# Kernel tuning notes

Measured on AMD Instinct MI355X. Metric: run time of the kernel, lower is better.

The kernel has to match this reference:

```python
import jax, jax.numpy as jnp
import numpy as np

N_NODES = 50000
N_EDGES = 800000
IN_DIM = 64


def setup_inputs() -> dict:
    key = jax.random.key(0)
    ks = jax.random.split(key, 5)
    h = jax.random.normal(ks[0], (N_NODES, IN_DIM), dtype=jnp.float32)
    src = jax.random.randint(ks[1], (N_EDGES,), 0, N_NODES, dtype=jnp.int64 if jax.config.read('jax_enable_x64') else jnp.int32)
    dst = jax.random.randint(ks[2], (N_EDGES,), 0, N_NODES, dtype=src.dtype)
    # attention MLP: Linear(2*in_dim, 1); stored as [2*in_dim, 1] (x @ W + b)
    W_att = jax.random.normal(ks[3], (2 * IN_DIM, 1), dtype=jnp.float32) / np.sqrt(2 * IN_DIM)
    b_att = jnp.zeros((1,), dtype=jnp.float32)
    W_t = jax.random.normal(ks[4], (IN_DIM, IN_DIM), dtype=jnp.float32) / np.sqrt(IN_DIM)
    b_t = jnp.zeros((IN_DIM,), dtype=jnp.float32)
    return {"h": h, "src": src, "dst": dst, "W_att": W_att, "b_att": b_att, "W_t": W_t, "b_t": b_t}


def reference(h, src, dst, W_att, b_att, W_t, b_t):
    h_src = h[src]                                   # [E, D] gather
    h_dst = h[dst]                                   # [E, D] gather
    edge_feat = jnp.concatenate([h_src, h_dst], axis=-1)  # [E, 2D]
    logits = jax.nn.leaky_relu(edge_feat @ W_att + b_att, negative_slope=0.2)[:, 0]  # [E]
    # NOTE: original does softmax over ALL edges globally (dim=0), not per-node
    attn = jax.nn.softmax(logits)                    # [E]
    msg = h_src * attn[:, None]                      # [E, D]
    h_agg = jnp.zeros_like(h).at[dst].add(msg)       # scatter-add [N, D]
    h_new = jax.nn.relu(h_agg @ W_t + b_t)           # transform + ReLU (dropout=eval identity)
    h_new = h_new + h                                # residual
    return (h_new, attn)
```

## Files before the change

### kernel.cpp

```cpp
#include <hip/hip_runtime.h>

#define N_NODES 50000
#define N_EDGES 800000
#define D 64
#define SCAN_BLOCKS ((N_NODES + 255) / 256)

__global__ __launch_bounds__(256) void node_proj(
    const float* __restrict__ h, const float* __restrict__ W_att,
    const float* __restrict__ b_att, float* __restrict__ a1, float* __restrict__ a2) {
    int gid  = blockIdx.x * blockDim.x + threadIdx.x;
    int node = gid >> 6;
    int lane = threadIdx.x & 63;
    if (node >= N_NODES) return;
    float x  = h[(size_t)node * D + lane];
    float p1 = x * W_att[lane];
    float p2 = x * W_att[64 + lane];
    #pragma unroll
    for (int o = 32; o; o >>= 1) {
        p1 += __shfl_down(p1, o);
        p2 += __shfl_down(p2, o);
    }
    if (lane == 0) {
        a1[node] = p1;
        a2[node] = p2 + b_att[0];
    }
}

__global__ __launch_bounds__(256) void edge_exp_hist(
    const int* __restrict__ src, const int* __restrict__ dst,
    const float* __restrict__ a1, const float* __restrict__ a2,
    float* __restrict__ p, unsigned* __restrict__ cnt, float* __restrict__ gsum) {
    __shared__ float red[256];
    float local = 0.0f;
    for (int e = blockIdx.x * 256 + threadIdx.x; e < N_EDGES; e += 512 * 256) {
        int s = src[e], d = dst[e];
        float v = a1[s] + a2[d];
        v = v > 0.0f ? v : 0.2f * v;
        float pe = __expf(v);
        p[e] = pe;
        local += pe;
        atomicAdd(&cnt[d], 1u);
    }
    red[threadIdx.x] = local;
    __syncthreads();
    for (int o = 128; o; o >>= 1) {
        if (threadIdx.x < o) red[threadIdx.x] += red[threadIdx.x + o];
        __syncthreads();
    }
    if (threadIdx.x == 0) atomicAdd(gsum, red[0]);
}

__global__ __launch_bounds__(256) void scanA(
    const unsigned* __restrict__ cnt, unsigned* __restrict__ local,
    unsigned* __restrict__ bsum) {
    __shared__ unsigned s[256];
    int i = blockIdx.x * 256 + threadIdx.x;
    unsigned v = (i < N_NODES) ? cnt[i] : 0u;
    s[threadIdx.x] = v;
    __syncthreads();
    for (int off = 1; off < 256; off <<= 1) {
        unsigned t = (threadIdx.x >= off) ? s[threadIdx.x - off] : 0u;
        __syncthreads();
        s[threadIdx.x] += t;
        __syncthreads();
    }
    if (i < N_NODES) local[i] = s[threadIdx.x] - v;
    if (threadIdx.x == 255) bsum[blockIdx.x] = s[255];
}

__global__ __launch_bounds__(256) void scanB(unsigned* __restrict__ bsum) {
    __shared__ unsigned s[256];
    unsigned v = (threadIdx.x < SCAN_BLOCKS) ? bsum[threadIdx.x] : 0u;
    s[threadIdx.x] = v;
    __syncthreads();
    for (int off = 1; off < 256; off <<= 1) {
        unsigned t = (threadIdx.x >= off) ? s[threadIdx.x - off] : 0u;
        __syncthreads();
        s[threadIdx.x] += t;
        __syncthreads();
    }
    if (threadIdx.x < SCAN_BLOCKS) bsum[threadIdx.x] = s[threadIdx.x] - v;
}

__global__ __launch_bounds__(256) void scanC(
    const unsigned* __restrict__ local, const unsigned* __restrict__ bsum,
    unsigned* __restrict__ row_start, unsigned* __restrict__ cursor) {
    int i = blockIdx.x * 256 + threadIdx.x;
    if (i >= N_NODES) return;
    unsigned r = local[i] + bsum[blockIdx.x];
    row_start[i] = r;
    cursor[i]    = r;
}

__global__ __launch_bounds__(256) void normalize_fill(
    const int* __restrict__ src, const int* __restrict__ dst,
    const float* __restrict__ p, const float* __restrict__ gsum,
    float* __restrict__ attn, unsigned* __restrict__ cursor,
    uint2* __restrict__ records) {
    int e = blockIdx.x * 256 + threadIdx.x;
    if (e >= N_EDGES) return;
    float a = p[e] / gsum[0];
    attn[e] = a;
    int d = dst[e];
    unsigned pos = atomicAdd(&cursor[d], 1u);
    records[pos] = make_uint2((unsigned)src[e], __float_as_uint(a));
}

__global__ __launch_bounds__(256) void gather_transform(
    const uint2* __restrict__ records, const unsigned* __restrict__ row_start,
    const unsigned* __restrict__ row_end, const float* __restrict__ h,
    const float* __restrict__ W_t, const float* __restrict__ b_t,
    float* __restrict__ out) {
    __shared__ float w[64 * 64];
    for (int i = threadIdx.x; i < 64 * 64; i += 256) w[i] = W_t[i];
    __syncthreads();
    int wave = threadIdx.x >> 6;
    int lane = threadIdx.x & 63;
    int n = blockIdx.x * 4 + wave;
    if (n >= N_NODES) return;

    int i0 = (int)row_start[n];
    int i1 = (int)row_end[n];
    float acc0 = 0.0f, acc1 = 0.0f;
    int i = i0;
    for (; i + 1 < i1; i += 2) {
        uint2 r0 = records[i];
        uint2 r1 = records[i + 1];
        acc0 = fmaf(h[(size_t)r0.x * D + lane], __uint_as_float(r0.y), acc0);
        acc1 = fmaf(h[(size_t)r1.x * D + lane], __uint_as_float(r1.y), acc1);
    }
    if (i < i1) {
        uint2 r = records[i];
        acc0 = fmaf(h[(size_t)r.x * D + lane], __uint_as_float(r.y), acc0);
    }
    float agg = acc0 + acc1;

    float o = b_t[lane];
    #pragma unroll
    for (int k = 0; k < 64; ++k)
        o = fmaf(__shfl(agg, k), w[k * 64 + lane], o);
    o = fmaxf(o, 0.0f);
    out[(size_t)n * D + lane] = o + h[(size_t)n * D + lane];
}

extern "C" void kernel_launch(void* const* d_in, const int* in_sizes, int n_in,
                              void* d_out, int out_size, void* d_ws, size_t ws_size,
                              hipStream_t stream) {
    const float* h     = (const float*)d_in[0];
    const int*   src   = (const int*)d_in[1];
    const int*   dst   = (const int*)d_in[2];
    const float* W_att = (const float*)d_in[3];
    const float* b_att = (const float*)d_in[4];
    const float* W_t   = (const float*)d_in[5];
    const float* b_t   = (const float*)d_in[6];

    float* h_new = (float*)d_out;
    float* attn  = (float*)d_out + (size_t)N_NODES * D;

    unsigned* cnt       = (unsigned*)d_ws;
    float*    gsum      = (float*)(cnt + N_NODES);
    float*    a1        = (float*)(cnt + N_NODES + 2);
    float*    a2        = a1 + N_NODES;
    unsigned* local     = (unsigned*)(a2 + N_NODES);
    unsigned* bsum      = local + N_NODES;
    unsigned* row_start = bsum + 256;
    unsigned* cursor    = row_start + N_NODES;
    float*    p         = (float*)(cursor + N_NODES);
    uint2*    records   = (uint2*)(p + N_EDGES);

    hipMemsetAsync(cnt, 0, (N_NODES + 2) * sizeof(unsigned), stream);

    node_proj<<<(N_NODES * 64 + 255) / 256, 256, 0, stream>>>(h, W_att, b_att, a1, a2);
    edge_exp_hist<<<512, 256, 0, stream>>>(src, dst, a1, a2, p, cnt, gsum);
    scanA<<<SCAN_BLOCKS, 256, 0, stream>>>(cnt, local, bsum);
    scanB<<<1, 256, 0, stream>>>(bsum);
    scanC<<<SCAN_BLOCKS, 256, 0, stream>>>(local, bsum, row_start, cursor);
    normalize_fill<<<(N_EDGES + 255) / 256, 256, 0, stream>>>(src, dst, p, gsum, attn, cursor, records);
    gather_transform<<<(N_NODES + 3) / 4, 256, 0, stream>>>(records, row_start, cursor, h, W_t, b_t, h_new);
}
```

Before: 272.3 us.

## Vectorize edge kernels, replace scan with atomic row allocation, split gather/transform

Edge kernels now process four edges per thread using int4/float4 loads and stores, and multiply by a precomputed reciprocal instead of dividing. The three-kernel prefix scan becomes a single kernel where each wave takes its row offsets from a global atomic counter. Rows stay contiguous per node but are no longer in node order, which is valid because the CSR only needs per-node ranges. The fused gather+transform is split into a 4-way unrolled gather writing h_agg into the output buffer, then a tiled LDS matmul kernel that handles 64 nodes per block with float4 outputs. This adds one extra round trip of h_agg through memory in exchange for fewer shuffles.

```diff
diff --git a/kernel.cpp b/kernel.cpp
--- a/kernel.cpp
+++ b/kernel.cpp
@@ -3,7 +3,6 @@
 #define N_NODES 50000
 #define N_EDGES 800000
 #define D 64
-#define SCAN_BLOCKS ((N_NODES + 255) / 256)
 
 __global__ __launch_bounds__(256) void node_proj(
     const float* __restrict__ h, const float* __restrict__ W_att,
@@ -27,19 +26,30 @@
 }
 
 __global__ __launch_bounds__(256) void edge_exp_hist(
-    const int* __restrict__ src, const int* __restrict__ dst,
+    const int4* __restrict__ src4, const int4* __restrict__ dst4,
     const float* __restrict__ a1, const float* __restrict__ a2,
-    float* __restrict__ p, unsigned* __restrict__ cnt, float* __restrict__ gsum) {
+    float4* __restrict__ p4, unsigned* __restrict__ cnt, float* __restrict__ gsum) {
     __shared__ float red[256];
+    int t = blockIdx.x * 256 + threadIdx.x;
     float local = 0.0f;
-    for (int e = blockIdx.x * 256 + threadIdx.x; e < N_EDGES; e += 512 * 256) {
-        int s = src[e], d = dst[e];
-        float v = a1[s] + a2[d];
-        v = v > 0.0f ? v : 0.2f * v;
-        float pe = __expf(v);
-        p[e] = pe;
-        local += pe;
-        atomicAdd(&cnt[d], 1u);
+    if (t < N_EDGES / 4) {
+        int4 s = src4[t];
+        int4 d = dst4[t];
+        float v0 = a1[s.x] + a2[d.x];
+        float v1 = a1[s.y] + a2[d.y];
+        float v2 = a1[s.z] + a2[d.z];
+        float v3 = a1[s.w] + a2[d.w];
+        v0 = v0 > 0.0f ? v0 : 0.2f * v0;
+        v1 = v1 > 0.0f ? v1 : 0.2f * v1;
+        v2 = v2 > 0.0f ? v2 : 0.2f * v2;
+        v3 = v3 > 0.0f ? v3 : 0.2f * v3;
+        float e0 = __expf(v0), e1 = __expf(v1), e2 = __expf(v2), e3 = __expf(v3);
+        p4[t] = make_float4(e0, e1, e2, e3);
+        local = (e0 + e1) + (e2 + e3);
+        atomicAdd(&cnt[d.x], 1u);
+        atomicAdd(&cnt[d.y], 1u);
+        atomicAdd(&cnt[d.z], 1u);
+        atomicAdd(&cnt[d.w], 1u);
     }
     red[threadIdx.x] = local;
     __syncthreads();
@@ -50,97 +60,140 @@
     if (threadIdx.x == 0) atomicAdd(gsum, red[0]);
 }
 
-__global__ __launch_bounds__(256) void scanA(
-    const unsigned* __restrict__ cnt, unsigned* __restrict__ local,
-    unsigned* __restrict__ bsum) {
-    __shared__ unsigned s[256];
-    int i = blockIdx.x * 256 + threadIdx.x;
+__global__ __launch_bounds__(256) void alloc_rows(
+    const unsigned* __restrict__ cnt, unsigned* __restrict__ row_start,
+    unsigned* __restrict__ cursor, unsigned* __restrict__ total) {
+    int i    = blockIdx.x * 256 + threadIdx.x;
+    int lane = threadIdx.x & 63;
     unsigned v = (i < N_NODES) ? cnt[i] : 0u;
-    s[threadIdx.x] = v;
-    __syncthreads();
-    for (int off = 1; off < 256; off <<= 1) {
-        unsigned t = (threadIdx.x >= off) ? s[threadIdx.x - off] : 0u;
-        __syncthreads();
-        s[threadIdx.x] += t;
-        __syncthreads();
-    }
-    if (i < N_NODES) local[i] = s[threadIdx.x] - v;
-    if (threadIdx.x == 255) bsum[blockIdx.x] = s[255];
-}
-
-__global__ __launch_bounds__(256) void scanB(unsigned* __restrict__ bsum) {
-    __shared__ unsigned s[256];
-    unsigned v = (threadIdx.x < SCAN_BLOCKS) ? bsum[threadIdx.x] : 0u;
-    s[threadIdx.x] = v;
-    __syncthreads();
-    for (int off = 1; off < 256; off <<= 1) {
-        unsigned t = (threadIdx.x >= off) ? s[threadIdx.x - off] : 0u;
-        __syncthreads();
-        s[threadIdx.x] += t;
-        __syncthreads();
-    }
-    if (threadIdx.x < SCAN_BLOCKS) bsum[threadIdx.x] = s[threadIdx.x] - v;
-}
-
-__global__ __launch_bounds__(256) void scanC(
-    const unsigned* __restrict__ local, const unsigned* __restrict__ bsum,
-    unsigned* __restrict__ row_start, unsigned* __restrict__ cursor) {
-    int i = blockIdx.x * 256 + threadIdx.x;
-    if (i >= N_NODES) return;
-    unsigned r = local[i] + bsum[blockIdx.x];
-    row_start[i] = r;
-    cursor[i]    = r;
+    unsigned incl = v;
+    #pragma unroll
+    for (int o = 1; o < 64; o <<= 1) {
+        unsigned u = __shfl_up(incl, o);
+        if (lane >= o) incl += u;
+    }
+    unsigned wsum = __shfl(incl, 63);
+    unsigned base = 0;
+    if (lane == 0) base = atomicAdd(total, wsum);
+    base = __shfl(base, 0);
+    if (i < N_NODES) {
+        unsigned r = base + incl - v;
+        row_start[i] = r;
+        cursor[i]    = r;
+    }
 }
 
 __global__ __launch_bounds__(256) void normalize_fill(
-    const int* __restrict__ src, const int* __restrict__ dst,
-    const float* __restrict__ p, const float* __restrict__ gsum,
-    float* __restrict__ attn, unsigned* __restrict__ cursor,
+    const int4* __restrict__ src4, const int4* __restrict__ dst4,
+    const float4* __restrict__ p4, const float* __restrict__ gsum,
+    float4* __restrict__ attn4, unsigned* __restrict__ cursor,
     uint2* __restrict__ records) {
-    int e = blockIdx.x * 256 + threadIdx.x;
-    if (e >= N_EDGES) return;
-    float a = p[e] / gsum[0];
-    attn[e] = a;
-    int d = dst[e];
-    unsigned pos = atomicAdd(&cursor[d], 1u);
-    records[pos] = make_uint2((unsigned)src[e], __float_as_uint(a));
-}
-
-__global__ __launch_bounds__(256) void gather_transform(
+    int t = blockIdx.x * 256 + threadIdx.x;
+    if (t >= N_EDGES / 4) return;
+    float inv = 1.0f / gsum[0];
+    int4   s = src4[t];
+    int4   d = dst4[t];
+    float4 p = p4[t];
+    float4 a = make_float4(p.x * inv, p.y * inv, p.z * inv, p.w * inv);
+    attn4[t] = a;
+    unsigned q0 = atomicAdd(&cursor[d.x], 1u);
+    records[q0] = make_uint2((unsigned)s.x, __float_as_uint(a.x));
+    unsigned q1 = atomicAdd(&cursor[d.y], 1u);
+    records[q1] = make_uint2((unsigned)s.y, __float_as_uint(a.y));
+    unsigned q2 = atomicAdd(&cursor[d.z], 1u);
+    records[q2] = make_uint2((unsigned)s.z, __float_as_uint(a.z));
+    unsigned q3 = atomicAdd(&cursor[d.w], 1u);
+    records[q3] = make_uint2((unsigned)s.w, __float_as_uint(a.w));
+}
+
+__global__ __launch_bounds__(256) void gather(
     const uint2* __restrict__ records, const unsigned* __restrict__ row_start,
     const unsigned* __restrict__ row_end, const float* __restrict__ h,
+    float* __restrict__ hagg) {
+    int gid  = blockIdx.x * blockDim.x + threadIdx.x;
+    int n    = gid >> 6;
+    int lane = threadIdx.x & 63;
+    if (n >= N_NODES) return;
+    int i  = (int)row_start[n];
+    int i1 = (int)row_end[n];
+    float c0 = 0.0f, c1 = 0.0f, c2 = 0.0f, c3 = 0.0f;
+    for (; i + 3 < i1; i += 4) {
+        uint2 r0 = records[i];
+        uint2 r1 = records[i + 1];
+        uint2 r2 = records[i + 2];
+        uint2 r3 = records[i + 3];
+        c0 = fmaf(h[(size_t)r0.x * D + lane], __uint_as_float(r0.y), c0);
+        c1 = fmaf(h[(size_t)r1.x * D + lane], __uint_as_float(r1.y), c1);
+        c2 = fmaf(h[(size_t)r2.x * D + lane], __uint_as_float(r2.y), c2);
+        c3 = fmaf(h[(size_t)r3.x * D + lane], __uint_as_float(r3.y), c3);
+    }
+    for (; i < i1; ++i) {
+        uint2 r = records[i];
+        c0 = fmaf(h[(size_t)r.x * D + lane], __uint_as_float(r.y), c0);
+    }
+    hagg[(size_t)n * D + lane] = (c0 + c1) + (c2 + c3);
+}
+
+__global__ __launch_bounds__(256) void transform(
+    const float* __restrict__ hagg, const float* __restrict__ h,
     const float* __restrict__ W_t, const float* __restrict__ b_t,
     float* __restrict__ out) {
     __shared__ float w[64 * 64];
-    for (int i = threadIdx.x; i < 64 * 64; i += 256) w[i] = W_t[i];
+    __shared__ float hl[64 * 65];
+    int t  = threadIdx.x;
+    int n0 = blockIdx.x * 64;
+    for (int i = t; i < 4096; i += 256) w[i] = W_t[i];
+    for (int i = t; i < 4096; i += 256) {
+        int n = i >> 6, k = i & 63;
+        int node = n0 + n;
+        hl[n * 65 + k] = (node < N_NODES) ? hagg[(size_t)node * D + k] : 0.0f;
+    }
     __syncthreads();
-    int wave = threadIdx.x >> 6;
-    int lane = threadIdx.x & 63;
-    int n = blockIdx.x * 4 + wave;
-    if (n >= N_NODES) return;
-
-    int i0 = (int)row_start[n];
-    int i1 = (int)row_end[n];
-    float acc0 = 0.0f, acc1 = 0.0f;
-    int i = i0;
-    for (; i + 1 < i1; i += 2) {
-        uint2 r0 = records[i];
-        uint2 r1 = records[i + 1];
-        acc0 = fmaf(h[(size_t)r0.x * D + lane], __uint_as_float(r0.y), acc0);
-        acc1 = fmaf(h[(size_t)r1.x * D + lane], __uint_as_float(r1.y), acc1);
-    }
-    if (i < i1) {
-        uint2 r = records[i];
-        acc0 = fmaf(h[(size_t)r.x * D + lane], __uint_as_float(r.y), acc0);
-    }
-    float agg = acc0 + acc1;
-
-    float o = b_t[lane];
-    #pragma unroll
-    for (int k = 0; k < 64; ++k)
-        o = fmaf(__shfl(agg, k), w[k * 64 + lane], o);
-    o = fmaxf(o, 0.0f);
-    out[(size_t)n * D + lane] = o + h[(size_t)n * D + lane];
+
+    int n    = t >> 2;
+    int j0   = (t & 3) * 16;
+    int node = n0 + n;
+    float4 acc0 = *(const float4*)&b_t[j0];
+    float4 acc1 = *(const float4*)&b_t[j0 + 4];
+    float4 acc2 = *(const float4*)&b_t[j0 + 8];
+    float4 acc3 = *(const float4*)&b_t[j0 + 12];
+    #pragma unroll 4
+    for (int k = 0; k < 64; ++k) {
+        float a = hl[n * 65 + k];
+        float4 w0 = *(const float4*)&w[k * 64 + j0];
+        float4 w1 = *(const float4*)&w[k * 64 + j0 + 4];
+        float4 w2 = *(const float4*)&w[k * 64 + j0 + 8];
+        float4 w3 = *(const float4*)&w[k * 64 + j0 + 12];
+        acc0.x = fmaf(a, w0.x, acc0.x); acc0.y = fmaf(a, w0.y, acc0.y);
+        acc0.z = fmaf(a, w0.z, acc0.z); acc0.w = fmaf(a, w0.w, acc0.w);
+        acc1.x = fmaf(a, w1.x, acc1.x); acc1.y = fmaf(a, w1.y, acc1.y);
+        acc1.z = fmaf(a, w1.z, acc1.z); acc1.w = fmaf(a, w1.w, acc1.w);
+        acc2.x = fmaf(a, w2.x, acc2.x); acc2.y = fmaf(a, w2.y, acc2.y);
+        acc2.z = fmaf(a, w2.z, acc2.z); acc2.w = fmaf(a, w2.w, acc2.w);
+        acc3.x = fmaf(a, w3.x, acc3.x); acc3.y = fmaf(a, w3.y, acc3.y);
+        acc3.z = fmaf(a, w3.z, acc3.z); acc3.w = fmaf(a, w3.w, acc3.w);
+    }
+    if (node < N_NODES) {
+        const float* hrow = &h[(size_t)node * D + j0];
+        float* orow = &out[(size_t)node * D + j0];
+        float4 h0 = *(const float4*)&hrow[0];
+        float4 h1 = *(const float4*)&hrow[4];
+        float4 h2 = *(const float4*)&hrow[8];
+        float4 h3 = *(const float4*)&hrow[12];
+        float4 o0, o1, o2, o3;
+        o0.x = fmaxf(acc0.x, 0.f) + h0.x; o0.y = fmaxf(acc0.y, 0.f) + h0.y;
+        o0.z = fmaxf(acc0.z, 0.f) + h0.z; o0.w = fmaxf(acc0.w, 0.f) + h0.w;
+        o1.x = fmaxf(acc1.x, 0.f) + h1.x; o1.y = fmaxf(acc1.y, 0.f) + h1.y;
+        o1.z = fmaxf(acc1.z, 0.f) + h1.z; o1.w = fmaxf(acc1.w, 0.f) + h1.w;
+        o2.x = fmaxf(acc2.x, 0.f) + h2.x; o2.y = fmaxf(acc2.y, 0.f) + h2.y;
+        o2.z = fmaxf(acc2.z, 0.f) + h2.z; o2.w = fmaxf(acc2.w, 0.f) + h2.w;
+        o3.x = fmaxf(acc3.x, 0.f) + h3.x; o3.y = fmaxf(acc3.y, 0.f) + h3.y;
+        o3.z = fmaxf(acc3.z, 0.f) + h3.z; o3.w = fmaxf(acc3.w, 0.f) + h3.w;
+        *(float4*)&orow[0]  = o0;
+        *(float4*)&orow[4]  = o1;
+        *(float4*)&orow[8]  = o2;
+        *(float4*)&orow[12] = o3;
+    }
 }
 
 extern "C" void kernel_launch(void* const* d_in, const int* in_sizes, int n_in,
@@ -156,25 +209,27 @@
 
     float* h_new = (float*)d_out;
     float* attn  = (float*)d_out + (size_t)N_NODES * D;
+    float* hagg  = h_new;
 
     unsigned* cnt       = (unsigned*)d_ws;
     float*    gsum      = (float*)(cnt + N_NODES);
-    float*    a1        = (float*)(cnt + N_NODES + 2);
+    unsigned* total     = (unsigned*)(gsum + 1);
+    float*    a1        = (float*)(total + 1);
     float*    a2        = a1 + N_NODES;
-    unsigned* local     = (unsigned*)(a2 + N_NODES);
-    unsigned* bsum      = local + N_NODES;
-    unsigned* row_start = bsum + 256;
+    unsigned* row_start = (unsigned*)(a2 + N_NODES);
     unsigned* cursor    = row_start + N_NODES;
     float*    p         = (float*)(cursor + N_NODES);
     uint2*    records   = (uint2*)(p + N_EDGES);
 
     hipMemsetAsync(cnt, 0, (N_NODES + 2) * sizeof(unsigned), stream);
 
-    node_proj<<<(N_NODES * 64 + 255) / 256, 256, 0, stream>>>(h, W_att, b_att, a1, a2);
-    edge_exp_hist<<<512, 256, 0, stream>>>(src, dst, a1, a2, p, cnt, gsum);
-    scanA<<<SCAN_BLOCKS, 256, 0, stream>>>(cnt, local, bsum);
-    scanB<<<1, 256, 0, stream>>>(bsum);
-    scanC<<<SCAN_BLOCKS, 256, 0, stream>>>(local, bsum, row_start, cursor);
-    normalize_fill<<<(N_EDGES + 255) / 256, 256, 0, stream>>>(src, dst, p, gsum, attn, cursor, records);
-    gather_transform<<<(N_NODES + 3) / 4, 256, 0, stream>>>(records, row_start, cursor, h, W_t, b_t, h_new);
-}
+    node_proj<<<(N_NODES * 64) / 256, 256, 0, stream>>>(h, W_att, b_att, a1, a2);
+    edge_exp_hist<<<(N_EDGES / 4 + 255) / 256, 256, 0, stream>>>(
+        (const int4*)src, (const int4*)dst, a1, a2, (float4*)p, cnt, gsum);
+    alloc_rows<<<(N_NODES + 255) / 256, 256, 0, stream>>>(cnt, row_start, cursor, total);
+    normalize_fill<<<(N_EDGES / 4 + 255) / 256, 256, 0, stream>>>(
+        (const int4*)src, (const int4*)dst, (const float4*)p, gsum,
+        (float4*)attn, cursor, records);
+    gather<<<(N_NODES * 64) / 256, 256, 0, stream>>>(records, row_start, cursor, h, hagg);
+    transform<<<(N_NODES + 63) / 64, 256, 0, stream>>>(hagg, h, W_t, b_t, h_new);
+}
```

Result: faster. 256.2 us (-5.9%).
